# Kernel optimization log

Measured on AMD Instinct MI355X. Metric: run time of the kernel, lower is better.

The kernel has to match this reference:

```python
import jax, jax.numpy as jnp
import numpy as np

B, S = 64, 1024
ATTEND_DIM = QUERY_DIM = ATT_DIM = 1024


def setup_inputs() -> dict:
    key = jax.random.key(0)
    ks = jax.random.split(key, 8)
    sc_pre = 1.0 / np.sqrt(ATTEND_DIM)
    sc_q = 1.0 / np.sqrt(QUERY_DIM)
    sc_v = 1.0 / np.sqrt(ATT_DIM)
    return {
        "input": jax.random.normal(ks[0], (B, QUERY_DIM), jnp.float32),
        "context": jax.random.normal(ks[1], (B, S, ATTEND_DIM), jnp.float32),
        "coverage_acc": jax.random.uniform(ks[2], (B, S), jnp.float32),
        "W_pre": jax.random.normal(ks[3], (ATT_DIM, ATTEND_DIM), jnp.float32) * sc_pre,
        "b_pre": jax.random.normal(ks[4], (ATT_DIM,), jnp.float32) * sc_pre,
        "W_q": jax.random.normal(ks[5], (ATT_DIM, QUERY_DIM), jnp.float32) * sc_q,
        "W_v": jax.random.normal(ks[6], (1, ATT_DIM), jnp.float32) * sc_v,
        "W_cov": jax.random.normal(ks[7], (ATT_DIM, 1), jnp.float32),
    }


def reference(input, context, coverage_acc, W_pre, b_pre, W_q, W_v, W_cov):
    # precompute = linear_pre(context): (B, S, att_dim)
    precompute = jnp.einsum('bsa,da->bsd', context, W_pre) + b_pre
    # targetT = linear_q(input): (B, 1, att_dim)
    targetT = (input @ W_q.T)[:, None, :]
    # coverage contribution: linear_cov(coverage[..., None]) -> (B, S, att_dim)
    cov_term = coverage_acc[..., None] * W_cov[:, 0]
    tmp = jnp.tanh(precompute + targetT + cov_term)
    # energy = linear_v(tanh(...)): (B, S)
    energy = jnp.einsum('bsd,d->bs', tmp, W_v[0])
    score = jax.nn.softmax(energy, axis=1)
    coverage_new = coverage_acc + score
    weightedContext = jnp.einsum('bs,bsa->ba', score, context)
    return (weightedContext, score, coverage_new, precompute)
```

## Files before the change

kernel.cpp:

```cpp
#include <hip/hip_runtime.h>
#include <hip/hip_bf16.h>

#define B_  64
#define S_  1024
#define D_  1024
#define K_  1024

typedef unsigned short u16;
typedef short bf16x8 __attribute__((ext_vector_type(8)));
typedef float f32x4  __attribute__((ext_vector_type(4)));
typedef u16   u16x8  __attribute__((ext_vector_type(8)));
typedef u16   u16x4  __attribute__((ext_vector_type(4)));

#define WS_TARGET 0
#define WS_EPART  262144
#define WS_WCPART 2359296
#define WS_WPRE   4456448
#define WS_CTXBF  6553600
#define WS_NEED_BF 140771328ull

__device__ __forceinline__ u16 f2bf(float f) {
    unsigned u = __float_as_uint(f);
    return (u16)((u + 0x7fffu + ((u >> 16) & 1u)) >> 16);
}

__device__ __forceinline__ float fast_tanh(float x) {
    float t = __expf(2.0f * x);
    return 1.0f - 2.0f * __builtin_amdgcn_rcpf(t + 1.0f);
}

__global__ void convert_bf16_kernel(const float* __restrict__ src, u16* __restrict__ dst) {
    size_t i = ((size_t)blockIdx.x * 256 + threadIdx.x) * 4;
    float4 v = *reinterpret_cast<const float4*>(src + i);
    u16x4 h = { f2bf(v.x), f2bf(v.y), f2bf(v.z), f2bf(v.w) };
    *reinterpret_cast<u16x4*>(dst + i) = h;
}

__global__ void target_kernel(const float* __restrict__ inp, const float* __restrict__ wq,
                              float* __restrict__ target) {
    int tid  = threadIdx.x;
    int lane = tid & 63, wid = tid >> 6;
    int pair = blockIdx.x * 4 + wid;
    int b = pair >> 10, n = pair & 1023;
    const float* ir = inp + (size_t)b * K_;
    const float* wr = wq  + (size_t)n * K_;
    float acc = 0.f;
#pragma unroll
    for (int jj = 0; jj < 4; ++jj) {
        int off = jj * 256 + lane * 4;
        float4 a = *reinterpret_cast<const float4*>(ir + off);
        float4 w = *reinterpret_cast<const float4*>(wr + off);
        acc += a.x * w.x + a.y * w.y + a.z * w.z + a.w * w.w;
    }
#pragma unroll
    for (int off = 1; off < 64; off <<= 1) acc += __shfl_xor(acc, off);
    if (lane == 0) target[pair] = acc;
}

#define LDA 40

template<bool CTXBF>
__global__ __launch_bounds__(256, 2)
void gemm_ep_kernel(const float* __restrict__ ctxf, const u16* __restrict__ ctxb,
                    const u16* __restrict__ wpre, const float* __restrict__ bpre,
                    const float* __restrict__ wv,  const float* __restrict__ wcov,
                    const float* __restrict__ target, const float* __restrict__ cov,
                    float* __restrict__ pre_out, float* __restrict__ epart) {
    __shared__ __align__(16) u16 As[256 * LDA];
    __shared__ __align__(16) u16 Bs[128 * LDA];
    __shared__ float esm[256];

    const int tid  = threadIdx.x;
    const int lane = tid & 63;
    const int wid  = tid >> 6;
    const int wm = wid >> 1, wn = wid & 1;
    const int lr = lane & 15, quad = lane >> 4;
    const int m_base = blockIdx.y * 256;
    const int n_base = blockIdx.x * 128;
    const int b      = m_base >> 10;
    const int s_base = m_base & 1023;

    f32x4 acc[8][4];
#pragma unroll
    for (int i = 0; i < 8; ++i)
#pragma unroll
        for (int j = 0; j < 4; ++j) acc[i][j] = (f32x4){0.f, 0.f, 0.f, 0.f};

    esm[tid] = 0.0f;

    for (int kt = 0; kt < 32; ++kt) {
        const int k0 = kt * 32;
        if constexpr (CTXBF) {
            const int row0 = tid >> 2, kc = (tid & 3) * 8;
#pragma unroll
            for (int p = 0; p < 4; ++p) {
                int row = row0 + p * 64;
                u16x8 v = *reinterpret_cast<const u16x8*>(
                    ctxb + (size_t)(m_base + row) * K_ + k0 + kc);
                *reinterpret_cast<u16x8*>(&As[row * LDA + kc]) = v;
            }
        } else {
            const int row0 = tid >> 3, kc = (tid & 7) * 4;
#pragma unroll
            for (int p = 0; p < 8; ++p) {
                int row = row0 + p * 32;
                float4 v = *reinterpret_cast<const float4*>(
                    ctxf + (size_t)(m_base + row) * K_ + k0 + kc);
                u16x4 h = { f2bf(v.x), f2bf(v.y), f2bf(v.z), f2bf(v.w) };
                *reinterpret_cast<u16x4*>(&As[row * LDA + kc]) = h;
            }
        }
        {
            const int row0 = tid >> 2, kc = (tid & 3) * 8;
#pragma unroll
            for (int p = 0; p < 2; ++p) {
                int row = row0 + p * 64;
                u16x8 v = *reinterpret_cast<const u16x8*>(
                    wpre + (size_t)(n_base + row) * K_ + k0 + kc);
                *reinterpret_cast<u16x8*>(&Bs[row * LDA + kc]) = v;
            }
        }
        __syncthreads();
        bf16x8 af[8], bf[4];
#pragma unroll
        for (int i = 0; i < 8; ++i)
            af[i] = *reinterpret_cast<const bf16x8*>(&As[(wm * 128 + i * 16 + lr) * LDA + quad * 8]);
#pragma unroll
        for (int j = 0; j < 4; ++j)
            bf[j] = *reinterpret_cast<const bf16x8*>(&Bs[(wn * 64 + j * 16 + lr) * LDA + quad * 8]);
#pragma unroll
        for (int i = 0; i < 8; ++i)
#pragma unroll
            for (int j = 0; j < 4; ++j)
                acc[i][j] = __builtin_amdgcn_mfma_f32_16x16x32_bf16(af[i], bf[j], acc[i][j], 0, 0, 0);
        __syncthreads();
    }

    float bpre_j[4], wv_j[4], wcov_j[4], tgt_j[4];
    int n_j[4];
#pragma unroll
    for (int j = 0; j < 4; ++j) {
        n_j[j]    = n_base + wn * 64 + j * 16 + lr;
        bpre_j[j] = bpre[n_j[j]];
        wv_j[j]   = wv[n_j[j]];
        wcov_j[j] = wcov[n_j[j]];
        tgt_j[j]  = target[b * D_ + n_j[j]];
    }
#pragma unroll
    for (int i = 0; i < 8; ++i) {
#pragma unroll
        for (int r = 0; r < 4; ++r) {
            int row_local = wm * 128 + i * 16 + quad * 4 + r;
            int m = m_base + row_local;
            int s = s_base + row_local;
            float c = cov[b * S_ + s];
            float esum = 0.f;
#pragma unroll
            for (int j = 0; j < 4; ++j) {
                float pre = acc[i][j][r] + bpre_j[j];
                pre_out[(size_t)m * D_ + n_j[j]] = pre;
                float t = fast_tanh(pre + tgt_j[j] + c * wcov_j[j]);
                esum += t * wv_j[j];
            }
            esum += __shfl_xor(esum, 1);
            esum += __shfl_xor(esum, 2);
            esum += __shfl_xor(esum, 4);
            esum += __shfl_xor(esum, 8);
            if (lr == 0) atomicAdd(&esm[row_local], esum);
        }
    }
    __syncthreads();
    epart[(size_t)(m_base + tid) * 8 + blockIdx.x] = esm[tid];
}

__global__ void softmax_cov_kernel(const float* __restrict__ epart, const float* __restrict__ cov,
                                   float* __restrict__ score, float* __restrict__ covnew) {
    int b = blockIdx.x, t = threadIdx.x;
    int lane = t & 63, wid = t >> 6;
    __shared__ float red[4];
    float e[4];
    float lmax = -3.4e38f;
#pragma unroll
    for (int p = 0; p < 4; ++p) {
        int s = p * 256 + t;
        const float4* q = reinterpret_cast<const float4*>(epart + (size_t)(b * S_ + s) * 8);
        float4 a = q[0], c = q[1];
        e[p] = a.x + a.y + a.z + a.w + c.x + c.y + c.z + c.w;
        lmax = fmaxf(lmax, e[p]);
    }
#pragma unroll
    for (int off = 1; off < 64; off <<= 1) lmax = fmaxf(lmax, __shfl_xor(lmax, off));
    if (lane == 0) red[wid] = lmax;
    __syncthreads();
    float bm = fmaxf(fmaxf(red[0], red[1]), fmaxf(red[2], red[3]));
    __syncthreads();
    float ex[4];
    float lsum = 0.f;
#pragma unroll
    for (int p = 0; p < 4; ++p) { ex[p] = __expf(e[p] - bm); lsum += ex[p]; }
#pragma unroll
    for (int off = 1; off < 64; off <<= 1) lsum += __shfl_xor(lsum, off);
    if (lane == 0) red[wid] = lsum;
    __syncthreads();
    float total = red[0] + red[1] + red[2] + red[3];
    float inv = __builtin_amdgcn_rcpf(total);
#pragma unroll
    for (int p = 0; p < 4; ++p) {
        int s = p * 256 + t;
        float sc = ex[p] * inv;
        score[b * S_ + s]  = sc;
        covnew[b * S_ + s] = cov[b * S_ + s] + sc;
    }
}

__global__ void wc_partial_kernel(const float* __restrict__ score, const float* __restrict__ ctx,
                                  float* __restrict__ part) {
    int sp = blockIdx.x, b = blockIdx.y, t = threadIdx.x;
    int col = t * 4;
    float ax = 0.f, ay = 0.f, az = 0.f, aw = 0.f;
    const float* base  = ctx + ((size_t)b * S_ + sp * 128) * K_ + col;
    const float* sbase = score + b * S_ + sp * 128;
    for (int ss = 0; ss < 128; ++ss) {
        float w = sbase[ss];
        float4 c = *reinterpret_cast<const float4*>(base + (size_t)ss * K_);
        ax += w * c.x; ay += w * c.y; az += w * c.z; aw += w * c.w;
    }
    float4 o = { ax, ay, az, aw };
    *reinterpret_cast<float4*>(part + (size_t)(b * 8 + sp) * 1024 + col) = o;
}

__global__ void wc_reduce_kernel(const float* __restrict__ part, float* __restrict__ wc) {
    int b = blockIdx.x, t = threadIdx.x;
    int col = t * 4;
    float ax = 0.f, ay = 0.f, az = 0.f, aw = 0.f;
#pragma unroll
    for (int p = 0; p < 8; ++p) {
        float4 v = *reinterpret_cast<const float4*>(part + (size_t)(b * 8 + p) * 1024 + col);
        ax += v.x; ay += v.y; az += v.z; aw += v.w;
    }
    float4 o = { ax, ay, az, aw };
    *reinterpret_cast<float4*>(wc + b * 1024 + col) = o;
}

extern "C" void kernel_launch(void* const* d_in, const int* in_sizes, int n_in,
                              void* d_out, int out_size, void* d_ws, size_t ws_size,
                              hipStream_t stream) {
    const float* input = (const float*)d_in[0];
    const float* ctx   = (const float*)d_in[1];
    const float* cov   = (const float*)d_in[2];
    const float* Wpre  = (const float*)d_in[3];
    const float* bpre  = (const float*)d_in[4];
    const float* Wq    = (const float*)d_in[5];
    const float* Wv    = (const float*)d_in[6];
    const float* Wcov  = (const float*)d_in[7];

    float* out        = (float*)d_out;
    float* out_wc     = out;
    float* out_score  = out + 65536;
    float* out_covnew = out + 131072;
    float* out_pre    = out + 196608;

    char*  ws        = (char*)d_ws;
    float* ws_target = (float*)(ws + WS_TARGET);
    float* ws_epart  = (float*)(ws + WS_EPART);
    float* ws_wcpart = (float*)(ws + WS_WCPART);
    u16*   ws_wpre   = (u16*)(ws + WS_WPRE);
    u16*   ws_ctxbf  = (u16*)(ws + WS_CTXBF);

    const bool use_ctx_bf = (ws_size >= WS_NEED_BF);

    convert_bf16_kernel<<<1024, 256, 0, stream>>>(Wpre, ws_wpre);
    if (use_ctx_bf)
        convert_bf16_kernel<<<65536, 256, 0, stream>>>(ctx, ws_ctxbf);
    target_kernel<<<16384, 256, 0, stream>>>(input, Wq, ws_target);
    dim3 ggrid(8, 256);
    if (use_ctx_bf)
        gemm_ep_kernel<true><<<ggrid, 256, 0, stream>>>(ctx, ws_ctxbf, ws_wpre, bpre, Wv, Wcov,
                                                        ws_target, cov, out_pre, ws_epart);
    else
        gemm_ep_kernel<false><<<ggrid, 256, 0, stream>>>(ctx, ws_ctxbf, ws_wpre, bpre, Wv, Wcov,
                                                         ws_target, cov, out_pre, ws_epart);
    softmax_cov_kernel<<<64, 256, 0, stream>>>(ws_epart, cov, out_score, out_covnew);
    wc_partial_kernel<<<dim3(8, 64), 256, 0, stream>>>(out_score, ctx, ws_wcpart);
    wc_reduce_kernel<<<64, 256, 0, stream>>>(ws_wcpart, out_wc);
}
```

Measured before the change: 786.9 us.

## Use direct global-to-LDS loads, bf16 weighted-context read, wider conversions and split

The bf16 GEMM path now stages A and B tiles with global_load_lds straight into unpadded shared memory instead of going through registers. The precompute output uses nontemporal stores, and the target layout is transposed. The conversion kernels handle 8 elements per thread. The weighted-context pass reads the bf16 copy of context instead of fp32 and is split into 16 partitions, which halves its memory traffic and adds parallelism at the cost of bf16 precision in the weighted context. The unpadded LDS layout may cause bank conflicts on the fragment reads.

```diff
diff --git a/kernel.cpp b/kernel.cpp
--- a/kernel.cpp
+++ b/kernel.cpp
@@ -15,25 +15,36 @@
 #define WS_TARGET 0
 #define WS_EPART  262144
 #define WS_WCPART 2359296
-#define WS_WPRE   4456448
-#define WS_CTXBF  6553600
-#define WS_NEED_BF 140771328ull
+#define WS_WPRE   6553600
+#define WS_CTXBF  8650752
+#define WS_NEED_BF 142868480ull
 
 __device__ __forceinline__ u16 f2bf(float f) {
     unsigned u = __float_as_uint(f);
     return (u16)((u + 0x7fffu + ((u >> 16) & 1u)) >> 16);
 }
-
+__device__ __forceinline__ float bf2f(u16 h) {
+    return __uint_as_float(((unsigned)h) << 16);
+}
 __device__ __forceinline__ float fast_tanh(float x) {
     float t = __expf(2.0f * x);
     return 1.0f - 2.0f * __builtin_amdgcn_rcpf(t + 1.0f);
 }
 
-__global__ void convert_bf16_kernel(const float* __restrict__ src, u16* __restrict__ dst) {
-    size_t i = ((size_t)blockIdx.x * 256 + threadIdx.x) * 4;
-    float4 v = *reinterpret_cast<const float4*>(src + i);
-    u16x4 h = { f2bf(v.x), f2bf(v.y), f2bf(v.z), f2bf(v.w) };
-    *reinterpret_cast<u16x4*>(dst + i) = h;
+__device__ __forceinline__ void glds16(const void* g, void* l) {
+    __builtin_amdgcn_global_load_lds(
+        (__attribute__((address_space(1))) void*)(size_t)g,
+        (__attribute__((address_space(3))) void*)(unsigned int)(size_t)l,
+        16, 0, 0);
+}
+
+__global__ void convert_bf16x8_kernel(const float* __restrict__ src, u16* __restrict__ dst) {
+    size_t i = ((size_t)blockIdx.x * 256 + threadIdx.x) * 8;
+    float4 a = *reinterpret_cast<const float4*>(src + i);
+    float4 b = *reinterpret_cast<const float4*>(src + i + 4);
+    u16x8 h = { f2bf(a.x), f2bf(a.y), f2bf(a.z), f2bf(a.w),
+                f2bf(b.x), f2bf(b.y), f2bf(b.z), f2bf(b.w) };
+    *reinterpret_cast<u16x8*>(dst + i) = h;
 }
 
 __global__ void target_kernel(const float* __restrict__ inp, const float* __restrict__ wq,
@@ -41,7 +52,7 @@
     int tid  = threadIdx.x;
     int lane = tid & 63, wid = tid >> 6;
     int pair = blockIdx.x * 4 + wid;
-    int b = pair >> 10, n = pair & 1023;
+    int b = pair & 63, n = pair >> 6;
     const float* ir = inp + (size_t)b * K_;
     const float* wr = wq  + (size_t)n * K_;
     float acc = 0.f;
@@ -57,17 +68,14 @@
     if (lane == 0) target[pair] = acc;
 }
 
-#define LDA 40
-
-template<bool CTXBF>
 __global__ __launch_bounds__(256, 2)
-void gemm_ep_kernel(const float* __restrict__ ctxf, const u16* __restrict__ ctxb,
-                    const u16* __restrict__ wpre, const float* __restrict__ bpre,
-                    const float* __restrict__ wv,  const float* __restrict__ wcov,
-                    const float* __restrict__ target, const float* __restrict__ cov,
-                    float* __restrict__ pre_out, float* __restrict__ epart) {
-    __shared__ __align__(16) u16 As[256 * LDA];
-    __shared__ __align__(16) u16 Bs[128 * LDA];
+void gemm_ep_fast(const u16* __restrict__ ctxb, const u16* __restrict__ wpre,
+                  const float* __restrict__ bpre, const float* __restrict__ wv,
+                  const float* __restrict__ wcov, const float* __restrict__ target,
+                  const float* __restrict__ cov, float* __restrict__ pre_out,
+                  float* __restrict__ epart) {
+    __shared__ __align__(16) u16 As[256 * 32];
+    __shared__ __align__(16) u16 Bs[128 * 32];
     __shared__ float esm[256];
 
     const int tid  = threadIdx.x;
@@ -80,6 +88,13 @@
     const int b      = m_base >> 10;
     const int s_base = m_base & 1023;
 
+    const int srow = lane >> 2;
+    const int scol = (lane & 3) * 8;
+    const u16* gA = ctxb + (size_t)(m_base + wid * 64 + srow) * K_ + scol;
+    const u16* gB = wpre + (size_t)(n_base + wid * 32 + srow) * K_ + scol;
+    u16* lA = &As[(wid * 64) * 32];
+    u16* lB = &Bs[(wid * 32) * 32];
+
     f32x4 acc[8][4];
 #pragma unroll
     for (int i = 0; i < 8; ++i)
@@ -90,16 +105,96 @@
 
     for (int kt = 0; kt < 32; ++kt) {
         const int k0 = kt * 32;
-        if constexpr (CTXBF) {
-            const int row0 = tid >> 2, kc = (tid & 3) * 8;
-#pragma unroll
-            for (int p = 0; p < 4; ++p) {
-                int row = row0 + p * 64;
-                u16x8 v = *reinterpret_cast<const u16x8*>(
-                    ctxb + (size_t)(m_base + row) * K_ + k0 + kc);
-                *reinterpret_cast<u16x8*>(&As[row * LDA + kc]) = v;
+#pragma unroll
+        for (int c = 0; c < 4; ++c)
+            glds16(gA + (size_t)(c * 16) * K_ + k0, lA + c * 16 * 32);
+#pragma unroll
+        for (int c = 0; c < 2; ++c)
+            glds16(gB + (size_t)(c * 16) * K_ + k0, lB + c * 16 * 32);
+        __syncthreads();
+
+        bf16x8 af[8], bfr[4];
+#pragma unroll
+        for (int i = 0; i < 8; ++i)
+            af[i] = *reinterpret_cast<const bf16x8*>(&As[(wm * 128 + i * 16 + lr) * 32 + quad * 8]);
+#pragma unroll
+        for (int j = 0; j < 4; ++j)
+            bfr[j] = *reinterpret_cast<const bf16x8*>(&Bs[(wn * 64 + j * 16 + lr) * 32 + quad * 8]);
+#pragma unroll
+        for (int i = 0; i < 8; ++i)
+#pragma unroll
+            for (int j = 0; j < 4; ++j)
+                acc[i][j] = __builtin_amdgcn_mfma_f32_16x16x32_bf16(af[i], bfr[j], acc[i][j], 0, 0, 0);
+        __syncthreads();
+    }
+
+    float bpre_j[4], wv_j[4], wcov_j[4], tgt_j[4];
+    int n_j[4];
+#pragma unroll
+    for (int j = 0; j < 4; ++j) {
+        n_j[j]    = n_base + wn * 64 + j * 16 + lr;
+        bpre_j[j] = bpre[n_j[j]];
+        wv_j[j]   = wv[n_j[j]];
+        wcov_j[j] = wcov[n_j[j]];
+        tgt_j[j]  = target[n_j[j] * 64 + b];
+    }
+#pragma unroll
+    for (int i = 0; i < 8; ++i) {
+#pragma unroll
+        for (int r = 0; r < 4; ++r) {
+            int row_local = wm * 128 + i * 16 + quad * 4 + r;
+            int m = m_base + row_local;
+            int s = s_base + row_local;
+            float c = cov[b * S_ + s];
+            float esum = 0.f;
+#pragma unroll
+            for (int j = 0; j < 4; ++j) {
+                float pre = acc[i][j][r] + bpre_j[j];
+                __builtin_nontemporal_store(pre, &pre_out[(size_t)m * D_ + n_j[j]]);
+                float t = fast_tanh(pre + tgt_j[j] + c * wcov_j[j]);
+                esum += t * wv_j[j];
             }
-        } else {
+            esum += __shfl_xor(esum, 1);
+            esum += __shfl_xor(esum, 2);
+            esum += __shfl_xor(esum, 4);
+            esum += __shfl_xor(esum, 8);
+            if (lr == 0) atomicAdd(&esm[row_local], esum);
+        }
+    }
+    __syncthreads();
+    epart[(size_t)(m_base + tid) * 8 + blockIdx.x] = esm[tid];
+}
+
+#define LDA 40
+__global__ __launch_bounds__(256, 2)
+void gemm_ep_fallback(const float* __restrict__ ctxf, const u16* __restrict__ wpre,
+                      const float* __restrict__ bpre, const float* __restrict__ wv,
+                      const float* __restrict__ wcov, const float* __restrict__ target,
+                      const float* __restrict__ cov, float* __restrict__ pre_out,
+                      float* __restrict__ epart) {
+    __shared__ __align__(16) u16 As[256 * LDA];
+    __shared__ __align__(16) u16 Bs[128 * LDA];
+    __shared__ float esm[256];
+    const int tid  = threadIdx.x;
+    const int lane = tid & 63;
+    const int wid  = tid >> 6;
+    const int wm = wid >> 1, wn = wid & 1;
+    const int lr = lane & 15, quad = lane >> 4;
+    const int m_base = blockIdx.y * 256;
+    const int n_base = blockIdx.x * 128;
+    const int b      = m_base >> 10;
+    const int s_base = m_base & 1023;
+
+    f32x4 acc[8][4];
+#pragma unroll
+    for (int i = 0; i < 8; ++i)
+#pragma unroll
+        for (int j = 0; j < 4; ++j) acc[i][j] = (f32x4){0.f, 0.f, 0.f, 0.f};
+    esm[tid] = 0.0f;
+
+    for (int kt = 0; kt < 32; ++kt) {
+        const int k0 = kt * 32;
+        {
             const int row0 = tid >> 3, kc = (tid & 7) * 4;
 #pragma unroll
             for (int p = 0; p < 8; ++p) {
@@ -121,21 +216,20 @@
             }
         }
         __syncthreads();
-        bf16x8 af[8], bf[4];
+        bf16x8 af[8], bfr[4];
 #pragma unroll
         for (int i = 0; i < 8; ++i)
             af[i] = *reinterpret_cast<const bf16x8*>(&As[(wm * 128 + i * 16 + lr) * LDA + quad * 8]);
 #pragma unroll
         for (int j = 0; j < 4; ++j)
-            bf[j] = *reinterpret_cast<const bf16x8*>(&Bs[(wn * 64 + j * 16 + lr) * LDA + quad * 8]);
+            bfr[j] = *reinterpret_cast<const bf16x8*>(&Bs[(wn * 64 + j * 16 + lr) * LDA + quad * 8]);
 #pragma unroll
         for (int i = 0; i < 8; ++i)
 #pragma unroll
             for (int j = 0; j < 4; ++j)
-                acc[i][j] = __builtin_amdgcn_mfma_f32_16x16x32_bf16(af[i], bf[j], acc[i][j], 0, 0, 0);
+                acc[i][j] = __builtin_amdgcn_mfma_f32_16x16x32_bf16(af[i], bfr[j], acc[i][j], 0, 0, 0);
         __syncthreads();
     }
-
     float bpre_j[4], wv_j[4], wcov_j[4], tgt_j[4];
     int n_j[4];
 #pragma unroll
@@ -144,7 +238,7 @@
         bpre_j[j] = bpre[n_j[j]];
         wv_j[j]   = wv[n_j[j]];
         wcov_j[j] = wcov[n_j[j]];
-        tgt_j[j]  = target[b * D_ + n_j[j]];
+        tgt_j[j]  = target[n_j[j] * 64 + b];
     }
 #pragma unroll
     for (int i = 0; i < 8; ++i) {
@@ -158,7 +252,7 @@
 #pragma unroll
             for (int j = 0; j < 4; ++j) {
                 float pre = acc[i][j][r] + bpre_j[j];
-                pre_out[(size_t)m * D_ + n_j[j]] = pre;
+                __builtin_nontemporal_store(pre, &pre_out[(size_t)m * D_ + n_j[j]]);
                 float t = fast_tanh(pre + tgt_j[j] + c * wcov_j[j]);
                 esum += t * wv_j[j];
             }
@@ -213,20 +307,37 @@
     }
 }
 
-__global__ void wc_partial_kernel(const float* __restrict__ score, const float* __restrict__ ctx,
-                                  float* __restrict__ part) {
+__global__ void wc_partial_bf(const float* __restrict__ score, const u16* __restrict__ ctxb,
+                              float* __restrict__ part) {
     int sp = blockIdx.x, b = blockIdx.y, t = threadIdx.x;
     int col = t * 4;
     float ax = 0.f, ay = 0.f, az = 0.f, aw = 0.f;
-    const float* base  = ctx + ((size_t)b * S_ + sp * 128) * K_ + col;
-    const float* sbase = score + b * S_ + sp * 128;
-    for (int ss = 0; ss < 128; ++ss) {
+    const u16*   base  = ctxb + ((size_t)b * S_ + sp * 64) * K_ + col;
+    const float* sbase = score + b * S_ + sp * 64;
+    for (int ss = 0; ss < 64; ++ss) {
+        float w = sbase[ss];
+        u16x4 c = *reinterpret_cast<const u16x4*>(base + (size_t)ss * K_);
+        ax += w * bf2f(c[0]); ay += w * bf2f(c[1]);
+        az += w * bf2f(c[2]); aw += w * bf2f(c[3]);
+    }
+    float4 o = { ax, ay, az, aw };
+    *reinterpret_cast<float4*>(part + (size_t)(b * 16 + sp) * 1024 + col) = o;
+}
+
+__global__ void wc_partial_f32(const float* __restrict__ score, const float* __restrict__ ctx,
+                               float* __restrict__ part) {
+    int sp = blockIdx.x, b = blockIdx.y, t = threadIdx.x;
+    int col = t * 4;
+    float ax = 0.f, ay = 0.f, az = 0.f, aw = 0.f;
+    const float* base  = ctx + ((size_t)b * S_ + sp * 64) * K_ + col;
+    const float* sbase = score + b * S_ + sp * 64;
+    for (int ss = 0; ss < 64; ++ss) {
         float w = sbase[ss];
         float4 c = *reinterpret_cast<const float4*>(base + (size_t)ss * K_);
         ax += w * c.x; ay += w * c.y; az += w * c.z; aw += w * c.w;
     }
     float4 o = { ax, ay, az, aw };
-    *reinterpret_cast<float4*>(part + (size_t)(b * 8 + sp) * 1024 + col) = o;
+    *reinterpret_cast<float4*>(part + (size_t)(b * 16 + sp) * 1024 + col) = o;
 }
 
 __global__ void wc_reduce_kernel(const float* __restrict__ part, float* __restrict__ wc) {
@@ -234,8 +345,8 @@
     int col = t * 4;
     float ax = 0.f, ay = 0.f, az = 0.f, aw = 0.f;
 #pragma unroll
-    for (int p = 0; p < 8; ++p) {
-        float4 v = *reinterpret_cast<const float4*>(part + (size_t)(b * 8 + p) * 1024 + col);
+    for (int p = 0; p < 16; ++p) {
+        float4 v = *reinterpret_cast<const float4*>(part + (size_t)(b * 16 + p) * 1024 + col);
         ax += v.x; ay += v.y; az += v.z; aw += v.w;
     }
     float4 o = { ax, ay, az, aw };
@@ -267,20 +378,23 @@
     u16*   ws_wpre   = (u16*)(ws + WS_WPRE);
     u16*   ws_ctxbf  = (u16*)(ws + WS_CTXBF);
 
-    const bool use_ctx_bf = (ws_size >= WS_NEED_BF);
-
-    convert_bf16_kernel<<<1024, 256, 0, stream>>>(Wpre, ws_wpre);
-    if (use_ctx_bf)
-        convert_bf16_kernel<<<65536, 256, 0, stream>>>(ctx, ws_ctxbf);
+    const bool use_bf = (ws_size >= WS_NEED_BF);
+
+    convert_bf16x8_kernel<<<512, 256, 0, stream>>>(Wpre, ws_wpre);
+    if (use_bf)
+        convert_bf16x8_kernel<<<32768, 256, 0, stream>>>(ctx, ws_ctxbf);
     target_kernel<<<16384, 256, 0, stream>>>(input, Wq, ws_target);
     dim3 ggrid(8, 256);
-    if (use_ctx_bf)
-        gemm_ep_kernel<true><<<ggrid, 256, 0, stream>>>(ctx, ws_ctxbf, ws_wpre, bpre, Wv, Wcov,
-                                                        ws_target, cov, out_pre, ws_epart);
+    if (use_bf)
+        gemm_ep_fast<<<ggrid, 256, 0, stream>>>(ws_ctxbf, ws_wpre, bpre, Wv, Wcov,
+                                                ws_target, cov, out_pre, ws_epart);
     else
-        gemm_ep_kernel<false><<<ggrid, 256, 0, stream>>>(ctx, ws_ctxbf, ws_wpre, bpre, Wv, Wcov,
-                                                         ws_target, cov, out_pre, ws_epart);
+        gemm_ep_fallback<<<ggrid, 256, 0, stream>>>(ctx, ws_wpre, bpre, Wv, Wcov,
+                                                    ws_target, cov, out_pre, ws_epart);
     softmax_cov_kernel<<<64, 256, 0, stream>>>(ws_epart, cov, out_score, out_covnew);
-    wc_partial_kernel<<<dim3(8, 64), 256, 0, stream>>>(out_score, ctx, ws_wcpart);
+    if (use_bf)
+        wc_partial_bf<<<dim3(16, 64), 256, 0, stream>>>(out_score, ws_ctxbf, ws_wcpart);
+    else
+        wc_partial_f32<<<dim3(16, 64), 256, 0, stream>>>(out_score, ctx, ws_wcpart);
     wc_reduce_kernel<<<64, 256, 0, stream>>>(ws_wcpart, out_wc);
 }
```

Result: faster. 696.5 us (-11.5%).
